# Performance work log

Measured on AMD Instinct MI355X. Metric: run time of the kernel, lower is better.

The kernel has to match this reference:

```python
import jax, jax.numpy as jnp
import numpy as np

B, S, T = 32, 64, 64          # batch, src_len, tgt_len
E, H, V = 512, 1024, 32000    # embed, hidden, vocab
WSCALE = 0.05                 # keep tanh/sigmoid in sane range


def setup_inputs() -> dict:
    key = jax.random.key(0)
    ks = jax.random.split(key, 14)
    n = lambda k, shp: jax.random.normal(k, shp, jnp.float32)
    return {
        "target": jax.random.randint(ks[0], (B, T), 0, V),
        "src_enc": n(ks[1], (B, S, 2 * H)),
        "h0": n(ks[2], (B, H)),
        "c0": n(ks[3], (B, H)),
        "emb": n(ks[4], (V, E)) * WSCALE,
        "W_ih": n(ks[5], (E, 4 * H)) * WSCALE,
        "W_hh": n(ks[6], (H, 4 * H)) * WSCALE,
        "b_rnn": jnp.zeros((4 * H,), jnp.float32),
        "W_attn": n(ks[7], (2 * H, H)) * WSCALE,
        "b_attn": jnp.zeros((H,), jnp.float32),
        "W_comb": n(ks[8], (2 * H, H)) * WSCALE,
        "b_comb": jnp.zeros((H,), jnp.float32),
        "W_out": n(ks[9], (H, V)) * WSCALE,
        "b_out": jnp.zeros((V,), jnp.float32),
    }


def reference(target, src_enc, h0, c0, emb, W_ih, W_hh, b_rnn,
              W_attn, b_attn, W_comb, b_comb, W_out, b_out):
    # Pre-project encoder states once (decode() applies attention.linear up front)
    enc_proj = src_enc @ W_attn + b_attn                 # [B,S,H]
    xs = emb[target[:, :-1]]                             # teacher forcing [B,T-1,E]
    xs = jnp.swapaxes(xs, 0, 1)                          # [T-1,B,E] for scan

    def step(carry, x_t):
        h, c = carry
        # LSTM cell (torch gate order i, f, g, o)
        gates = x_t @ W_ih + h @ W_hh + b_rnn            # [B,4H]
        i, f, g, o = jnp.split(gates, 4, axis=-1)
        c = jax.nn.sigmoid(f) * c + jax.nn.sigmoid(i) * jnp.tanh(g)
        h = jax.nn.sigmoid(o) * jnp.tanh(c)
        # Bilinear attention: score = h^T (W_attn e_s) over source positions
        scores = jnp.einsum('bsh,bh->bs', enc_proj, h)
        attn = jax.nn.softmax(scores, axis=-1)
        ctx = jnp.einsum('bs,bsh->bh', attn, enc_proj)   # [B,H]
        out = jnp.tanh(jnp.concatenate([h, ctx], axis=-1) @ W_comb + b_comb)
        return (h, c), out

    _, outs = jax.lax.scan(step, (h0, c0), xs)           # [T-1,B,H]
    outs = jnp.swapaxes(outs, 0, 1)                      # [B,T-1,H]
    logits = outs @ W_out + b_out                        # [B,T-1,V]
    return logits
```

## Files before the change

### kernel.cpp

```cpp
#include <hip/hip_runtime.h>
#include <stdint.h>

#define NB    32
#define NS    64
#define TDEC  63
#define NE    512
#define NH    1024
#define NV    32000

typedef float  floatx4 __attribute__((ext_vector_type(4)));
typedef short  short8  __attribute__((ext_vector_type(8)));
typedef short  short4v __attribute__((ext_vector_type(4)));

__device__ __forceinline__ float bf2f(short s) {
  return __uint_as_float(((uint32_t)(uint16_t)s) << 16);
}
__device__ __forceinline__ short f2bf(float f) {
  uint32_t u = __float_as_uint(f);
  uint32_t r = (u + 0x7fffu + ((u >> 16) & 1u)) >> 16;
  return (short)(uint16_t)r;
}
__device__ __forceinline__ float sigm(float x) { return 1.f / (1.f + expf(-x)); }

__device__ __forceinline__ int xcd_swz(int orig, int nwg) {
  return (orig & 7) * (nwg >> 3) + (orig >> 3);
}

__device__ __forceinline__ void tr_plain(
    const float* __restrict__ W, short* __restrict__ Wt, int K, int N,
    int bx, int by, int perm, float (*tile)[33], int tid)
{
  int k0 = bx * 32, n0 = by * 32;
  int tx = tid & 31, ty = tid >> 5;
#pragma unroll
  for (int r = 0; r < 32; r += 8)
    tile[ty + r][tx] = W[(size_t)(k0 + ty + r) * N + n0 + tx];
  __syncthreads();
  int kq = tid & 7, nl = tid >> 3;
  int n = n0 + nl;
  int rr = perm ? ((n & 1023) * 4 + (n >> 10)) : n;
  short4v v;
#pragma unroll
  for (int q = 0; q < 4; ++q) v[q] = f2bf(tile[kq * 4 + q][nl]);
  *(short4v*)&Wt[(size_t)rr * K + k0 + kq * 4] = v;
}

__device__ __forceinline__ void tr_split(
    const float* __restrict__ W, short* __restrict__ Wt_hi, short* __restrict__ Wt_lo,
    int K, int N, int bx, int by, int perm, float (*tile)[33], int tid)
{
  int k0 = bx * 32, n0 = by * 32;
  int tx = tid & 31, ty = tid >> 5;
#pragma unroll
  for (int r = 0; r < 32; r += 8)
    tile[ty + r][tx] = W[(size_t)(k0 + ty + r) * N + n0 + tx];
  __syncthreads();
  int kq = tid & 7, nl = tid >> 3;
  int n = n0 + nl;
  int rr = perm ? ((n & 1023) * 4 + (n >> 10)) : n;
  short4v vh, vl;
#pragma unroll
  for (int q = 0; q < 4; ++q) {
    float v = tile[kq * 4 + q][nl];
    short h = f2bf(v);
    vh[q] = h;
    vl[q] = f2bf(v - bf2f(h));
  }
  size_t o = (size_t)rr * K + k0 + kq * 4;
  *(short4v*)&Wt_hi[o] = vh;
  *(short4v*)&Wt_lo[o] = vl;
}

__global__ __launch_bounds__(256) void prep_all(
    const float* __restrict__ Wattn, const float* __restrict__ Wih,
    const float* __restrict__ Whh,
    const int* __restrict__ target,  const float* __restrict__ emb,
    const float* __restrict__ h0,    const float* __restrict__ c0,
    const float* __restrict__ brnn,  const float* __restrict__ src,
    short* __restrict__ WattnTh, short* __restrict__ WattnTl,
    short* __restrict__ WihTp,
    short* __restrict__ WhpHi,   short* __restrict__ WhpLo,
    short* __restrict__ xs, float* __restrict__ hf_all,
    short* __restrict__ hhi_all, short* __restrict__ hlo_all,
    float* __restrict__ c_buf, float* __restrict__ brnn_p,
    short* __restrict__ sAh, short* __restrict__ sAl)
{
  __shared__ float tile[32][33];
  const int blk = blockIdx.x;
  const int tid = threadIdx.x;

  if (blk < 2048) {
    tr_split(Wattn, WattnTh, WattnTl, 2048, 1024, blk & 63, blk >> 6, 0, tile, tid);
  } else if (blk < 4096) {
    int b = blk - 2048;
    tr_plain(Wih, WihTp, 512, 4096, b & 15, b >> 4, 1, tile, tid);
  } else if (blk < 8192) {
    int b = blk - 4096;
    tr_split(Whh, WhpHi, WhpLo, 1024, 4096, b & 31, b >> 5, 1, tile, tid);
  } else {
    const int NXS = TDEC * NB * NE;
    const int HN = NH * NB;
    const int NSRC = 2048 * 2048;
    int total = NXS + 2 * HN + 4096 + NSRC;
    int b = blk - 8192;
    for (int idx = b * 256 + tid; idx < total; idx += 2048 * 256) {
      if (idx < NXS) {
        int row = idx >> 9, e = idx & 511;
        int t = row >> 5, bb = row & 31;
        int token = target[bb * 64 + t];
        xs[idx] = f2bf(emb[(size_t)token * NE + e]);
      } else if (idx < NXS + HN) {
        int r = idx - NXS;
        float v = h0[r];
        hf_all[r] = v;
        short hh = f2bf(v);
        hhi_all[r] = hh;
        hlo_all[r] = f2bf(v - bf2f(hh));
      } else if (idx < NXS + 2 * HN) {
        int r = idx - NXS - HN;
        c_buf[r] = c0[r];
      } else if (idx < NXS + 2 * HN + 4096) {
        int c = idx - NXS - 2 * HN;
        brnn_p[c] = brnn[(c & 3) * 1024 + (c >> 2)];
      } else {
        int e = idx - NXS - 2 * HN - 4096;
        float v = src[e];
        short h = f2bf(v);
        sAh[e] = h;
        sAl[e] = f2bf(v - bf2f(h));
      }
    }
  }
}

template<int OUT_BF, int SWZ>
__global__ __launch_bounds__(256) void gemm_kernel(
    const short* __restrict__ Ab, const short* __restrict__ Bt,
    void* __restrict__ Cptr, const float* __restrict__ bias,
    int M, int N, int K)
{
  __shared__ char smem[2 * 128 * 72 * 2];
  short* As = (short*)smem;
  short* Bs = (short*)(smem + 128 * 72 * 2);
  float* cst = (float*)smem;
  int tile_id = blockIdx.y * gridDim.x + blockIdx.x;
  if (SWZ) tile_id = xcd_swz(tile_id, gridDim.x * gridDim.y);
  const int m0 = (tile_id % gridDim.x) * 128;
  const int n0 = (tile_id / gridDim.x) * 128;
  const int tid = threadIdx.x;
  const int lane = tid & 63;
  const int wid = tid >> 6;
  const int wr = wid >> 1, wc = wid & 1;

  floatx4 acc[4][4] = {};
  const int row = tid >> 1;
  const int ks  = (tid & 1) << 5;

  for (int k0 = 0; k0 < K; k0 += 64) {
    {
      int gm = m0 + row;
      short8 v0, v1, v2, v3;
      if (gm < M) {
        const short* src = Ab + (size_t)gm * K + k0 + ks;
        v0 = *(const short8*)src;
        v1 = *(const short8*)(src + 8);
        v2 = *(const short8*)(src + 16);
        v3 = *(const short8*)(src + 24);
      } else {
#pragma unroll
        for (int c = 0; c < 8; ++c) { v0[c] = 0; v1[c] = 0; v2[c] = 0; v3[c] = 0; }
      }
      *(short8*)&As[row * 72 + ks]      = v0;
      *(short8*)&As[row * 72 + ks + 8]  = v1;
      *(short8*)&As[row * 72 + ks + 16] = v2;
      *(short8*)&As[row * 72 + ks + 24] = v3;
    }
    {
      const short* src = Bt + (size_t)(n0 + row) * K + k0 + ks;
      *(short8*)&Bs[row * 72 + ks]      = *(const short8*)src;
      *(short8*)&Bs[row * 72 + ks + 8]  = *(const short8*)(src + 8);
      *(short8*)&Bs[row * 72 + ks + 16] = *(const short8*)(src + 16);
      *(short8*)&Bs[row * 72 + ks + 24] = *(const short8*)(src + 24);
    }
    __syncthreads();

    const int kA = (lane >> 4) << 3;
    const int rsel = lane & 15;
#pragma unroll
    for (int kk = 0; kk < 64; kk += 32) {
      short8 af[4], bfr[4];
#pragma unroll
      for (int mi = 0; mi < 4; ++mi)
        af[mi] = *(const short8*)&As[(wr * 64 + mi * 16 + rsel) * 72 + kk + kA];
#pragma unroll
      for (int ni = 0; ni < 4; ++ni)
        bfr[ni] = *(const short8*)&Bs[(wc * 64 + ni * 16 + rsel) * 72 + kk + kA];
#pragma unroll
      for (int mi = 0; mi < 4; ++mi)
#pragma unroll
        for (int ni = 0; ni < 4; ++ni)
          acc[mi][ni] = __builtin_amdgcn_mfma_f32_16x16x32_bf16(af[mi], bfr[ni], acc[mi][ni], 0, 0, 0);
    }
    __syncthreads();
  }

  const int crow = (lane >> 4) * 4;
  const int ccol = lane & 15;
  if (OUT_BF) {
#pragma unroll
    for (int mi = 0; mi < 4; ++mi) {
#pragma unroll
      for (int ni = 0; ni < 4; ++ni) {
        int gn = n0 + wc * 64 + ni * 16 + ccol;
        float bv = bias[gn];
#pragma unroll
        for (int i = 0; i < 4; ++i) {
          int gm = m0 + wr * 64 + mi * 16 + crow + i;
          if (gm < M)
            __builtin_nontemporal_store(f2bf(acc[mi][ni][i] + bv),
                                        &((short*)Cptr)[(size_t)gm * N + gn]);
        }
      }
    }
  } else {
#pragma unroll
    for (int p = 0; p < 4; ++p) {
      __syncthreads();
      if (wr == (p >> 1)) {
        int mi0 = (p & 1) * 2;
#pragma unroll
        for (int mm = 0; mm < 2; ++mm) {
#pragma unroll
          for (int ni = 0; ni < 4; ++ni) {
            int c = wc * 64 + ni * 16 + ccol;
#pragma unroll
            for (int i = 0; i < 4; ++i)
              cst[(mm * 16 + crow + i) * 132 + c] = acc[mi0 + mm][ni][i];
          }
        }
      }
      __syncthreads();
#pragma unroll
      for (int rep = 0; rep < 4; ++rep) {
        int cell = tid + rep * 256;
        int r = cell >> 5, q = cell & 31;
        int gm = m0 + p * 32 + r;
        int gn = n0 + q * 4;
        if (gm < M) {
          float4 bv = *(const float4*)&bias[gn];
          floatx4 v;
          v[0] = cst[r * 132 + q * 4 + 0] + bv.x;
          v[1] = cst[r * 132 + q * 4 + 1] + bv.y;
          v[2] = cst[r * 132 + q * 4 + 2] + bv.z;
          v[3] = cst[r * 132 + q * 4 + 3] + bv.w;
          __builtin_nontemporal_store(v, (floatx4*)&((float*)Cptr)[(size_t)gm * N + gn]);
        }
      }
    }
  }
}

__global__ __launch_bounds__(256) void gemm_pre(
    const short* __restrict__ Ah, const short* __restrict__ Al,
    const short* __restrict__ Bt_hi, const short* __restrict__ Bt_lo,
    float* __restrict__ Cenc, const float* __restrict__ battn,
    const short* __restrict__ Ag, const short* __restrict__ Btg,
    short* __restrict__ Cg, const float* __restrict__ brnn_p)
{
  __shared__ char smem[4 * 128 * 72 * 2];
  const int tid = threadIdx.x;
  const int lane = tid & 63;
  const int wid = tid >> 6;
  const int wr = wid >> 1, wc = wid & 1;
  const int row = tid >> 1;
  const int ks  = (tid & 1) << 5;
  const int kA = (lane >> 4) << 3;
  const int rsel = lane & 15;
  const int crow = (lane >> 4) * 4;
  const int ccol = lane & 15;

  if (blockIdx.x < 128) {
    short* As_hi = (short*)smem;
    short* As_lo = (short*)(smem + 1 * 128 * 72 * 2);
    short* Bs_hi = (short*)(smem + 2 * 128 * 72 * 2);
    short* Bs_lo = (short*)(smem + 3 * 128 * 72 * 2);
    const int K = 2048, N = NH;
    int tile_id = xcd_swz(blockIdx.x, 128);
    const int m0 = (tile_id % 16) * 128;
    const int n0 = (tile_id / 16) * 128;

    floatx4 acc[4][4] = {};
    for (int k0 = 0; k0 < K; k0 += 64) {
      {
        size_t o = (size_t)(m0 + row) * K + k0 + ks;
#pragma unroll
        for (int c = 0; c < 4; ++c) {
          *(short8*)&As_hi[row * 72 + ks + c * 8] = *(const short8*)(Ah + o + c * 8);
          *(short8*)&As_lo[row * 72 + ks + c * 8] = *(const short8*)(Al + o + c * 8);
        }
      }
      {
        size_t o = (size_t)(n0 + row) * K + k0 + ks;
#pragma unroll
        for (int c = 0; c < 4; ++c) {
          *(short8*)&Bs_hi[row * 72 + ks + c * 8] = *(const short8*)(Bt_hi + o + c * 8);
          *(short8*)&Bs_lo[row * 72 + ks + c * 8] = *(const short8*)(Bt_lo + o + c * 8);
        }
      }
      __syncthreads();
#pragma unroll
      for (int kk = 0; kk < 64; kk += 32) {
        short8 ah[4], al[4], bh[4], bl[4];
#pragma unroll
        for (int mi = 0; mi < 4; ++mi) {
          int off = (wr * 64 + mi * 16 + rsel) * 72 + kk + kA;
          ah[mi] = *(const short8*)&As_hi[off];
          al[mi] = *(const short8*)&As_lo[off];
        }
#pragma unroll
        for (int ni = 0; ni < 4; ++ni) {
          int off = (wc * 64 + ni * 16 + rsel) * 72 + kk + kA;
          bh[ni] = *(const short8*)&Bs_hi[off];
          bl[ni] = *(const short8*)&Bs_lo[off];
        }
#pragma unroll
        for (int mi = 0; mi < 4; ++mi)
#pragma unroll
          for (int ni = 0; ni < 4; ++ni) {
            floatx4 a = acc[mi][ni];
            a = __builtin_amdgcn_mfma_f32_16x16x32_bf16(al[mi], bh[ni], a, 0, 0, 0);
            a = __builtin_amdgcn_mfma_f32_16x16x32_bf16(ah[mi], bl[ni], a, 0, 0, 0);
            a = __builtin_amdgcn_mfma_f32_16x16x32_bf16(ah[mi], bh[ni], a, 0, 0, 0);
            acc[mi][ni] = a;
          }
      }
      __syncthreads();
    }
#pragma unroll
    for (int mi = 0; mi < 4; ++mi) {
#pragma unroll
      for (int ni = 0; ni < 4; ++ni) {
        int gn = n0 + wc * 64 + ni * 16 + ccol;
        float bv = battn[gn];
#pragma unroll
        for (int i = 0; i < 4; ++i) {
          int gm = m0 + wr * 64 + mi * 16 + crow + i;
          Cenc[(size_t)gm * N + gn] = acc[mi][ni][i] + bv;
        }
      }
    }
  } else {
    short* As = (short*)smem;
    short* Bs = (short*)(smem + 128 * 72 * 2);
    const int K = NE, N = 4096, M = TDEC * NB;
    int tile_id = xcd_swz(blockIdx.x - 128, 512);
    const int m0 = (tile_id % 16) * 128;
    const int n0 = (tile_id / 16) * 128;

    floatx4 acc[4][4] = {};
    for (int k0 = 0; k0 < K; k0 += 64) {
      {
        int gm = m0 + row;
        short8 v0, v1, v2, v3;
        if (gm < M) {
          const short* src = Ag + (size_t)gm * K + k0 + ks;
          v0 = *(const short8*)src;
          v1 = *(const short8*)(src + 8);
          v2 = *(const short8*)(src + 16);
          v3 = *(const short8*)(src + 24);
        } else {
#pragma unroll
          for (int c = 0; c < 8; ++c) { v0[c] = 0; v1[c] = 0; v2[c] = 0; v3[c] = 0; }
        }
        *(short8*)&As[row * 72 + ks]      = v0;
        *(short8*)&As[row * 72 + ks + 8]  = v1;
        *(short8*)&As[row * 72 + ks + 16] = v2;
        *(short8*)&As[row * 72 + ks + 24] = v3;
      }
      {
        const short* src = Btg + (size_t)(n0 + row) * K + k0 + ks;
        *(short8*)&Bs[row * 72 + ks]      = *(const short8*)src;
        *(short8*)&Bs[row * 72 + ks + 8]  = *(const short8*)(src + 8);
        *(short8*)&Bs[row * 72 + ks + 16] = *(const short8*)(src + 16);
        *(short8*)&Bs[row * 72 + ks + 24] = *(const short8*)(src + 24);
      }
      __syncthreads();
#pragma unroll
      for (int kk = 0; kk < 64; kk += 32) {
        short8 af[4], bfr[4];
#pragma unroll
        for (int mi = 0; mi < 4; ++mi)
          af[mi] = *(const short8*)&As[(wr * 64 + mi * 16 + rsel) * 72 + kk + kA];
#pragma unroll
        for (int ni = 0; ni < 4; ++ni)
          bfr[ni] = *(const short8*)&Bs[(wc * 64 + ni * 16 + rsel) * 72 + kk + kA];
#pragma unroll
        for (int mi = 0; mi < 4; ++mi)
#pragma unroll
          for (int ni = 0; ni < 4; ++ni)
            acc[mi][ni] = __builtin_amdgcn_mfma_f32_16x16x32_bf16(af[mi], bfr[ni], acc[mi][ni], 0, 0, 0);
      }
      __syncthreads();
    }
#pragma unroll
    for (int mi = 0; mi < 4; ++mi) {
#pragma unroll
      for (int ni = 0; ni < 4; ++ni) {
        int gn = n0 + wc * 64 + ni * 16 + ccol;
        float bv = brnn_p[gn];
#pragma unroll
        for (int i = 0; i < 4; ++i) {
          int gm = m0 + wr * 64 + mi * 16 + crow + i;
          if (gm < M)
            __builtin_nontemporal_store(f2bf(acc[mi][ni][i] + bv),
                                        &Cg[(size_t)gm * N + gn]);
        }
      }
    }
  }
}

__global__ __launch_bounds__(512) void scan_a(
    int t,
    const short* __restrict__ Whp_hi,
    const short* __restrict__ Whp_lo,
    const short* __restrict__ gatesx,
    short* __restrict__ hhi_all,
    short* __restrict__ hlo_all,
    float* __restrict__ hf_all,
    float* __restrict__ c_buf,
    const float* __restrict__ Wout,  short* __restrict__ WoutT,
    const float* __restrict__ Wcomb, short* __restrict__ WcTHi,
    short* __restrict__ WcTLo)
{
  __shared__ float smem[8 * 32 * 33];
  const int blk = blockIdx.x;
  const int tid = threadIdx.x;

  if (blk >= 128) {
    float (*tile)[33] = (float(*)[33])smem;
    if (blk < 636) {
      int id = t * 508 + (blk - 128);
      if (id < 32000) {
        int k0 = (id & 31) * 32, n0 = (id >> 5) * 32;
        if (tid < 256) {
          int tx = tid & 31, ty = tid >> 5;
#pragma unroll
          for (int r = 0; r < 32; r += 8)
            tile[ty + r][tx] = Wout[(size_t)(k0 + ty + r) * 32000 + n0 + tx];
        }
        __syncthreads();
        if (tid < 256) {
          int kq = tid & 7, nl = tid >> 3;
          int n = n0 + nl;
          short4v v;
#pragma unroll
          for (int q = 0; q < 4; ++q) v[q] = f2bf(tile[kq * 4 + q][nl]);
          *(short4v*)&WoutT[(size_t)n * 1024 + k0 + kq * 4] = v;
        }
      }
    } else {
      int id = t * 33 + (blk - 636);
      if (id < 2048) {
        int k0 = (id & 63) * 32, n0 = (id >> 6) * 32;
        if (tid < 256) {
          int tx = tid & 31, ty = tid >> 5;
#pragma unroll
          for (int r = 0; r < 32; r += 8)
            tile[ty + r][tx] = Wcomb[(size_t)(k0 + ty + r) * 1024 + n0 + tx];
        }
        __syncthreads();
        if (tid < 256) {
          int kq = tid & 7, nl = tid >> 3;
          int n = n0 + nl;
          short4v vh, vl;
#pragma unroll
          for (int q = 0; q < 4; ++q) {
            float v = tile[kq * 4 + q][nl];
            short h = f2bf(v);
            vh[q] = h;
            vl[q] = f2bf(v - bf2f(h));
          }
          size_t o = (size_t)n * 2048 + k0 + kq * 4;
          *(short4v*)&WcTHi[o] = vh;
          *(short4v*)&WcTLo[o] = vl;
        }
      }
    }
    return;
  }

  const int lane = tid & 63;
  const int wid = tid >> 6;
  const int rsel = lane & 15;
  const int kA = (lane >> 4) * 8;
  const int crow = (lane >> 4) * 4;
  const int ccol = lane & 15;

  const size_t spv = (size_t)t * (NH * NB);
  const size_t snw = (size_t)(t + 1) * (NH * NB);
  const short* Hh = hhi_all + spv;
  const short* Hl = hlo_all + spv;
  const int c0 = blk * 32;
  const int kb = wid * 128;

  floatx4 acc[2][2] = {};
  const short* wh0 = Whp_hi + (size_t)(c0 + rsel) * NH + kb + kA;
  const short* wl0 = Whp_lo + (size_t)(c0 + rsel) * NH + kb + kA;
  const short* wh1 = Whp_hi + (size_t)(c0 + 16 + rsel) * NH + kb + kA;
  const short* wl1 = Whp_lo + (size_t)(c0 + 16 + rsel) * NH + kb + kA;
  const short* ha0 = Hh + (size_t)rsel * NH + kb + kA;
  const short* la0 = Hl + (size_t)rsel * NH + kb + kA;
  const short* ha1 = Hh + (size_t)(16 + rsel) * NH + kb + kA;
  const short* la1 = Hl + (size_t)(16 + rsel) * NH + kb + kA;
#pragma unroll
  for (int kk = 0; kk < 4; ++kk) {
    int k0 = kk * 32;
    short8 a0h = *(const short8*)(ha0 + k0);
    short8 a0l = *(const short8*)(la0 + k0);
    short8 a1h = *(const short8*)(ha1 + k0);
    short8 a1l = *(const short8*)(la1 + k0);
    short8 b0h = *(const short8*)(wh0 + k0);
    short8 b0l = *(const short8*)(wl0 + k0);
    short8 b1h = *(const short8*)(wh1 + k0);
    short8 b1l = *(const short8*)(wl1 + k0);
    acc[0][0] = __builtin_amdgcn_mfma_f32_16x16x32_bf16(a0l, b0h, acc[0][0], 0, 0, 0);
    acc[0][0] = __builtin_amdgcn_mfma_f32_16x16x32_bf16(a0h, b0l, acc[0][0], 0, 0, 0);
    acc[0][0] = __builtin_amdgcn_mfma_f32_16x16x32_bf16(a0h, b0h, acc[0][0], 0, 0, 0);
    acc[0][1] = __builtin_amdgcn_mfma_f32_16x16x32_bf16(a0l, b1h, acc[0][1], 0, 0, 0);
    acc[0][1] = __builtin_amdgcn_mfma_f32_16x16x32_bf16(a0h, b1l, acc[0][1], 0, 0, 0);
    acc[0][1] = __builtin_amdgcn_mfma_f32_16x16x32_bf16(a0h, b1h, acc[0][1], 0, 0, 0);
    acc[1][0] = __builtin_amdgcn_mfma_f32_16x16x32_bf16(a1l, b0h, acc[1][0], 0, 0, 0);
    acc[1][0] = __builtin_amdgcn_mfma_f32_16x16x32_bf16(a1h, b0l, acc[1][0], 0, 0, 0);
    acc[1][0] = __builtin_amdgcn_mfma_f32_16x16x32_bf16(a1h, b0h, acc[1][0], 0, 0, 0);
    acc[1][1] = __builtin_amdgcn_mfma_f32_16x16x32_bf16(a1l, b1h, acc[1][1], 0, 0, 0);
    acc[1][1] = __builtin_amdgcn_mfma_f32_16x16x32_bf16(a1h, b1l, acc[1][1], 0, 0, 0);
    acc[1][1] = __builtin_amdgcn_mfma_f32_16x16x32_bf16(a1h, b1h, acc[1][1], 0, 0, 0);
  }
#pragma unroll
  for (int mi = 0; mi < 2; ++mi)
#pragma unroll
    for (int ni = 0; ni < 2; ++ni)
#pragma unroll
      for (int i = 0; i < 4; ++i)
        smem[wid * 1056 + (mi * 16 + crow + i) * 33 + ni * 16 + ccol] = acc[mi][ni][i];
  __syncthreads();
  if (tid < 256) {
    int b = tid & 31, jl = tid >> 5;
    float g[4];
#pragma unroll
    for (int q = 0; q < 4; ++q) {
      float s = 0;
#pragma unroll
      for (int w = 0; w < 8; ++w) s += smem[w * 1056 + b * 33 + jl * 4 + q];
      g[q] = s;
    }
    int jg = (c0 >> 2) + jl;
    const short* gx = gatesx + ((size_t)t * 32 + b) * 4096 + c0 + jl * 4;
    short4v gxv = *(const short4v*)gx;
    float gi = g[0] + bf2f(gxv[0]);
    float gf = g[1] + bf2f(gxv[1]);
    float gg = g[2] + bf2f(gxv[2]);
    float go = g[3] + bf2f(gxv[3]);
    float co = c_buf[b * NH + jg];
    float cn = sigm(gf) * co + sigm(gi) * tanhf(gg);
    float hn = sigm(go) * tanhf(cn);
    c_buf[b * NH + jg] = cn;
    hf_all[snw + b * NH + jg] = hn;
    short hh = f2bf(hn);
    hhi_all[snw + b * NH + jg] = hh;
    hlo_all[snw + b * NH + jg] = f2bf(hn - bf2f(hh));
  }
}

__global__ __launch_bounds__(256) void attn_batch(
    const float* __restrict__ encp,
    const float* __restrict__ hf_all,
    short* __restrict__ ctxhi_all,
    short* __restrict__ ctxlo_all)
{
  __shared__ float h_lds[NH];
  __shared__ float part[4 * 64];
  __shared__ float sc_lds[64];
  __shared__ float p_lds[64];
  const int blk = xcd_swz(blockIdx.x, gridDim.x);
  const int b = blk / TDEC;
  const int t = blk % TDEC;
  const int tid = threadIdx.x;
  const float* h = hf_all + ((size_t)(t + 1) * 32 + b) * NH;

  ((float4*)h_lds)[tid] = ((const float4*)h)[tid];
  __syncthreads();
  {
    int s = tid & 63, kc = tid >> 6;
    const float4* ep = (const float4*)(encp + ((size_t)(b * 64 + s)) * NH + kc * 256);
    const float4* hp = (const float4*)(h_lds + kc * 256);
    float ac0 = 0, ac1 = 0, ac2 = 0, ac3 = 0;
#pragma unroll
    for (int i = 0; i < 64; i += 4) {
      float4 e0 = ep[i],     h0v = hp[i];
      float4 e1 = ep[i + 1], h1v = hp[i + 1];
      float4 e2 = ep[i + 2], h2v = hp[i + 2];
      float4 e3 = ep[i + 3], h3v = hp[i + 3];
      ac0 = fmaf(e0.x, h0v.x, ac0); ac0 = fmaf(e0.y, h0v.y, ac0);
      ac0 = fmaf(e0.z, h0v.z, ac0); ac0 = fmaf(e0.w, h0v.w, ac0);
      ac1 = fmaf(e1.x, h1v.x, ac1); ac1 = fmaf(e1.y, h1v.y, ac1);
      ac1 = fmaf(e1.z, h1v.z, ac1); ac1 = fmaf(e1.w, h1v.w, ac1);
      ac2 = fmaf(e2.x, h2v.x, ac2); ac2 = fmaf(e2.y, h2v.y, ac2);
      ac2 = fmaf(e2.z, h2v.z, ac2); ac2 = fmaf(e2.w, h2v.w, ac2);
      ac3 = fmaf(e3.x, h3v.x, ac3); ac3 = fmaf(e3.y, h3v.y, ac3);
      ac3 = fmaf(e3.z, h3v.z, ac3); ac3 = fmaf(e3.w, h3v.w, ac3);
    }
    part[kc * 64 + s] = (ac0 + ac1) + (ac2 + ac3);
  }
  __syncthreads();
  if (tid < 64) {
    float sc = part[tid] + part[64 + tid] + part[128 + tid] + part[192 + tid];
    sc_lds[tid] = sc;
    float m = sc;
#pragma unroll
    for (int off = 32; off; off >>= 1) m = fmaxf(m, __shfl_xor(m, off));
    float e = expf(sc - m);
    float sum = e;
#pragma unroll
    for (int off = 32; off; off >>= 1) sum += __shfl_xor(sum, off);
    p_lds[tid] = e / sum;
  }
  __syncthreads();
  {
    int k4 = tid * 4;
    float a0 = 0, a1 = 0, a2 = 0, a3 = 0;
    const float* ep = encp + (size_t)(b * 64) * NH + k4;
    for (int s = 0; s < 64; ++s) {
      float p = p_lds[s];
      float4 e = *(const float4*)(ep + (size_t)s * NH);
      a0 = fmaf(p, e.x, a0); a1 = fmaf(p, e.y, a1);
      a2 = fmaf(p, e.z, a2); a3 = fmaf(p, e.w, a3);
    }
    size_t crow = ((size_t)t * 32 + b) * NH + k4;
    short4v c4h, c4l;
    float av[4] = {a0, a1, a2, a3};
#pragma unroll
    for (int q = 0; q < 4; ++q) {
      short hh = f2bf(av[q]);
      c4h[q] = hh;
      c4l[q] = f2bf(av[q] - bf2f(hh));
    }
    *(short4v*)(ctxhi_all + crow) = c4h;
    *(short4v*)(ctxlo_all + crow) = c4l;
  }
}

__global__ __launch_bounds__(256) void gemm_comb(
    const short* __restrict__ Ah_hi,
    const short* __restrict__ Ah_lo,
    const short* __restrict__ Cx_hi,
    const short* __restrict__ Cx_lo,
    const short* __restrict__ Bt_hi,
    const short* __restrict__ Bt_lo,
    const float* __restrict__ bcomb,
    short* __restrict__ outs)
{
  __shared__ short As_hi[128 * 72];
  __shared__ short As_lo[128 * 72];
  __shared__ short Bs_hi[128 * 72];
  __shared__ short Bs_lo[128 * 72];
  int tile_id = xcd_swz(blockIdx.y * gridDim.x + blockIdx.x, gridDim.x * gridDim.y);
  const int m0 = (tile_id % gridDim.x) * 128;
  const int n0 = (tile_id / gridDim.x) * 128;
  const int tid = threadIdx.x;
  const int lane = tid & 63;
  const int wid = tid >> 6;
  const int wr = wid >> 1, wc = wid & 1;

  floatx4 acc[4][4] = {};
  const int row = tid >> 1;
  const int ks  = (tid & 1) << 5;

  for (int k0 = 0; k0 < 2048; k0 += 64) {
    {
      int gr = m0 + row;
      const short* sh;
      const short* sl;
      if (k0 < NH) {
        sh = Ah_hi + (size_t)gr * NH + k0 + ks;
        sl = Ah_lo + (size_t)gr * NH + k0 + ks;
      } else {
        sh = Cx_hi + (size_t)gr * NH + (k0 - NH) + ks;
        sl = Cx_lo + (size_t)gr * NH + (k0 - NH) + ks;
      }
#pragma unroll
      for (int c = 0; c < 4; ++c) {
        *(short8*)&As_hi[row * 72 + ks + c * 8] = *(const short8*)(sh + c * 8);
        *(short8*)&As_lo[row * 72 + ks + c * 8] = *(const short8*)(sl + c * 8);
      }
    }
    {
      size_t o = (size_t)(n0 + row) * 2048 + k0 + ks;
#pragma unroll
      for (int c = 0; c < 4; ++c) {
        *(short8*)&Bs_hi[row * 72 + ks + c * 8] = *(const short8*)(Bt_hi + o + c * 8);
        *(short8*)&Bs_lo[row * 72 + ks + c * 8] = *(const short8*)(Bt_lo + o + c * 8);
      }
    }
    __syncthreads();

    const int kA = (lane >> 4) << 3;
    const int rsel = lane & 15;
#pragma unroll
    for (int kk = 0; kk < 64; kk += 32) {
      short8 ah[4], al[4], bh[4], bl[4];
#pragma unroll
      for (int mi = 0; mi < 4; ++mi) {
        int off = (wr * 64 + mi * 16 + rsel) * 72 + kk + kA;
        ah[mi] = *(const short8*)&As_hi[off];
        al[mi] = *(const short8*)&As_lo[off];
      }
#pragma unroll
      for (int ni = 0; ni < 4; ++ni) {
        int off = (wc * 64 + ni * 16 + rsel) * 72 + kk + kA;
        bh[ni] = *(const short8*)&Bs_hi[off];
        bl[ni] = *(const short8*)&Bs_lo[off];
      }
#pragma unroll
      for (int mi = 0; mi < 4; ++mi)
#pragma unroll
        for (int ni = 0; ni < 4; ++ni) {
          floatx4 a = acc[mi][ni];
          a = __builtin_amdgcn_mfma_f32_16x16x32_bf16(al[mi], bh[ni], a, 0, 0, 0);
          a = __builtin_amdgcn_mfma_f32_16x16x32_bf16(ah[mi], bl[ni], a, 0, 0, 0);
          a = __builtin_amdgcn_mfma_f32_16x16x32_bf16(ah[mi], bh[ni], a, 0, 0, 0);
          acc[mi][ni] = a;
        }
    }
    __syncthreads();
  }

  const int crow = (lane >> 4) * 4;
  const int ccol = lane & 15;
#pragma unroll
  for (int mi = 0; mi < 4; ++mi) {
#pragma unroll
    for (int ni = 0; ni < 4; ++ni) {
      int gn = n0 + wc * 64 + ni * 16 + ccol;
      float bv = bcomb[gn];
#pragma unroll
      for (int i = 0; i < 4; ++i) {
        int gm = m0 + wr * 64 + mi * 16 + crow + i;
        if (gm < TDEC * NB) {
          int tt = gm >> 5, bb = gm & 31;
          outs[((size_t)bb * TDEC + tt) * NH + gn] = f2bf(tanhf(acc[mi][ni][i] + bv));
        }
      }
    }
  }
}

extern "C" void kernel_launch(void* const* d_in, const int* in_sizes, int n_in,
                              void* d_out, int out_size, void* d_ws, size_t ws_size,
                              hipStream_t stream)
{
  const int*   target = (const int*)  d_in[0];
  const float* src    = (const float*)d_in[1];
  const float* h0     = (const float*)d_in[2];
  const float* c0     = (const float*)d_in[3];
  const float* emb    = (const float*)d_in[4];
  const float* Wih    = (const float*)d_in[5];
  const float* Whh    = (const float*)d_in[6];
  const float* brnn   = (const float*)d_in[7];
  const float* Wattn  = (const float*)d_in[8];
  const float* battn  = (const float*)d_in[9];
  const float* Wcomb  = (const float*)d_in[10];
  const float* bcomb  = (const float*)d_in[11];
  const float* Wout   = (const float*)d_in[12];
  const float* bout   = (const float*)d_in[13];
  float* out = (float*)d_out;

  char* ws = (char*)d_ws;
  size_t off = 0;
  auto take = [&](size_t bytes) { char* p = ws + off; off += (bytes + 255) & ~(size_t)255; return p; };
  short* WoutT    = (short*)take((size_t)NV * NH * 2);
  short* WattnTh  = (short*)take((size_t)NH * 2048 * 2);
  short* WattnTl  = (short*)take((size_t)NH * 2048 * 2);
  short* WihTp    = (short*)take((size_t)4096 * NE * 2);
  short* WhpHi    = (short*)take((size_t)4096 * NH * 2);
  short* WhpLo    = (short*)take((size_t)4096 * NH * 2);
  short* WcTHi    = (short*)take((size_t)NH * 2048 * 2);
  short* WcTLo    = (short*)take((size_t)NH * 2048 * 2);
  short* xs_bf    = (short*)take((size_t)TDEC * NB * NE * 2);
  float* encp     = (float*)take((size_t)NB * NS * NH * 4);
  short* gatesx   = (short*)take((size_t)TDEC * NB * 4096 * 2);
  short* outs_bf  = (short*)take((size_t)TDEC * NB * NH * 2);
  float* hf_all   = (float*)take((size_t)65 * NB * NH * 4);
  short* hhi_all  = (short*)take((size_t)65 * NB * NH * 2);
  short* hlo_all  = (short*)take((size_t)65 * NB * NH * 2);
  short* ctxhi_a  = (short*)take((size_t)2048 * NH * 2);
  short* ctxlo_a  = (short*)take((size_t)2048 * NH * 2);
  float* c_buf    = (float*)take((size_t)NH * NB * 4);
  float* brnn_p   = (float*)take((size_t)4096 * 4);
  short* sAl      = (short*)take((size_t)2048 * 2048 * 2);
  short* sAh      = (short*)take((size_t)2048 * 2048 * 2);
  if (off > ws_size) return;

  prep_all<<<10240, 256, 0, stream>>>(
      Wattn, Wih, Whh, target, emb, h0, c0, brnn, src,
      WattnTh, WattnTl, WihTp, WhpHi, WhpLo,
      xs_bf, hf_all, hhi_all, hlo_all, c_buf, brnn_p, sAh, sAl);
  gemm_pre<<<640, 256, 0, stream>>>(
      sAh, sAl, WattnTh, WattnTl, encp, battn,
      xs_bf, WihTp, gatesx, brnn_p);
  for (int t = 0; t < TDEC; ++t)
    scan_a<<<669, 512, 0, stream>>>(t, WhpHi, WhpLo, gatesx, hhi_all, hlo_all,
                                    hf_all, c_buf, Wout, WoutT, Wcomb, WcTHi, WcTLo);
  attn_batch<<<TDEC * NB, 256, 0, stream>>>(encp, hf_all, ctxhi_a, ctxlo_a);
  gemm_comb<<<dim3(16, 8), 256, 0, stream>>>(hhi_all + (size_t)32 * NH, hlo_all + (size_t)32 * NH,
                                             ctxhi_a, ctxlo_a, WcTHi, WcTLo, bcomb, outs_bf);
  gemm_kernel<0, 1><<<dim3(16, NV / 128), 256, 0, stream>>>(outs_bf, WoutT, out, bout, TDEC * NB, NV, NH);
}
```

Before: 1.137 ms.

## Fuse attention into scan launches, lagging one step behind the LSTM recurrence

Removes the separate batched attention kernel and computes each step's attention in 32 extra blocks of the scan launch, using the hidden state from the previous launch (t-1). An extra 64th launch finishes the last attention step. The aim is to hide attention work inside the latency-bound serial scan launches, where many CUs sit idle. In exchange it adds one more kernel launch, and the attention blocks now compete with the recurrence blocks in every step.

```diff
diff --git a/kernel.cpp b/kernel.cpp
--- a/kernel.cpp
+++ b/kernel.cpp
@@ -431,16 +431,91 @@
     float* __restrict__ c_buf,
     const float* __restrict__ Wout,  short* __restrict__ WoutT,
     const float* __restrict__ Wcomb, short* __restrict__ WcTHi,
-    short* __restrict__ WcTLo)
+    short* __restrict__ WcTLo,
+    const float* __restrict__ encp,
+    short* __restrict__ ctxhi_all,
+    short* __restrict__ ctxlo_all)
 {
   __shared__ float smem[8 * 32 * 33];
   const int blk = blockIdx.x;
   const int tid = threadIdx.x;
 
-  if (blk >= 128) {
+  if (blk >= 128 && blk < 160) {
+    const int ta = t - 1;
+    if (ta < 0 || ta >= TDEC) return;
+    const int b = blk - 128;
+    float* h_lds  = smem;
+    float* part   = smem + 1024;
+    float* sc_lds = smem + 1280;
+    float* p_lds  = smem + 1344;
+    const float* h = hf_all + ((size_t)(ta + 1) * 32 + b) * NH;
+    if (tid < 256) ((float4*)h_lds)[tid] = ((const float4*)h)[tid];
+    __syncthreads();
+    if (tid < 256) {
+      int s = tid & 63, kc = tid >> 6;
+      const float4* ep = (const float4*)(encp + ((size_t)(b * 64 + s)) * NH + kc * 256);
+      const float4* hp = (const float4*)(h_lds + kc * 256);
+      float ac0 = 0, ac1 = 0, ac2 = 0, ac3 = 0;
+#pragma unroll
+      for (int i = 0; i < 64; i += 4) {
+        float4 e0 = ep[i],     h0v = hp[i];
+        float4 e1 = ep[i + 1], h1v = hp[i + 1];
+        float4 e2 = ep[i + 2], h2v = hp[i + 2];
+        float4 e3 = ep[i + 3], h3v = hp[i + 3];
+        ac0 = fmaf(e0.x, h0v.x, ac0); ac0 = fmaf(e0.y, h0v.y, ac0);
+        ac0 = fmaf(e0.z, h0v.z, ac0); ac0 = fmaf(e0.w, h0v.w, ac0);
+        ac1 = fmaf(e1.x, h1v.x, ac1); ac1 = fmaf(e1.y, h1v.y, ac1);
+        ac1 = fmaf(e1.z, h1v.z, ac1); ac1 = fmaf(e1.w, h1v.w, ac1);
+        ac2 = fmaf(e2.x, h2v.x, ac2); ac2 = fmaf(e2.y, h2v.y, ac2);
+        ac2 = fmaf(e2.z, h2v.z, ac2); ac2 = fmaf(e2.w, h2v.w, ac2);
+        ac3 = fmaf(e3.x, h3v.x, ac3); ac3 = fmaf(e3.y, h3v.y, ac3);
+        ac3 = fmaf(e3.z, h3v.z, ac3); ac3 = fmaf(e3.w, h3v.w, ac3);
+      }
+      part[kc * 64 + s] = (ac0 + ac1) + (ac2 + ac3);
+    }
+    __syncthreads();
+    if (tid < 64) {
+      float sc = part[tid] + part[64 + tid] + part[128 + tid] + part[192 + tid];
+      sc_lds[tid] = sc;
+      float m = sc;
+#pragma unroll
+      for (int off = 32; off; off >>= 1) m = fmaxf(m, __shfl_xor(m, off));
+      float e = expf(sc - m);
+      float sum = e;
+#pragma unroll
+      for (int off = 32; off; off >>= 1) sum += __shfl_xor(sum, off);
+      p_lds[tid] = e / sum;
+    }
+    __syncthreads();
+    if (tid < 256) {
+      int k4 = tid * 4;
+      float a0 = 0, a1 = 0, a2 = 0, a3 = 0;
+      const float* ep = encp + (size_t)(b * 64) * NH + k4;
+      for (int s = 0; s < 64; ++s) {
+        float p = p_lds[s];
+        float4 e = *(const float4*)(ep + (size_t)s * NH);
+        a0 = fmaf(p, e.x, a0); a1 = fmaf(p, e.y, a1);
+        a2 = fmaf(p, e.z, a2); a3 = fmaf(p, e.w, a3);
+      }
+      size_t crow2 = ((size_t)ta * 32 + b) * NH + k4;
+      short4v c4h, c4l;
+      float av[4] = {a0, a1, a2, a3};
+#pragma unroll
+      for (int q = 0; q < 4; ++q) {
+        short hh = f2bf(av[q]);
+        c4h[q] = hh;
+        c4l[q] = f2bf(av[q] - bf2f(hh));
+      }
+      *(short4v*)(ctxhi_all + crow2) = c4h;
+      *(short4v*)(ctxlo_all + crow2) = c4l;
+    }
+    return;
+  }
+
+  if (blk >= 160) {
     float (*tile)[33] = (float(*)[33])smem;
-    if (blk < 636) {
-      int id = t * 508 + (blk - 128);
+    if (blk < 668) {
+      int id = t * 508 + (blk - 160);
       if (id < 32000) {
         int k0 = (id & 31) * 32, n0 = (id >> 5) * 32;
         if (tid < 256) {
@@ -460,7 +535,7 @@
         }
       }
     } else {
-      int id = t * 33 + (blk - 636);
+      int id = t * 33 + (blk - 668);
       if (id < 2048) {
         int k0 = (id & 63) * 32, n0 = (id >> 6) * 32;
         if (tid < 256) {
@@ -490,6 +565,7 @@
     return;
   }
 
+  if (t >= TDEC) return;
   const int lane = tid & 63;
   const int wid = tid >> 6;
   const int rsel = lane & 15;
@@ -570,84 +646,6 @@
     short hh = f2bf(hn);
     hhi_all[snw + b * NH + jg] = hh;
     hlo_all[snw + b * NH + jg] = f2bf(hn - bf2f(hh));
-  }
-}
-
-__global__ __launch_bounds__(256) void attn_batch(
-    const float* __restrict__ encp,
-    const float* __restrict__ hf_all,
-    short* __restrict__ ctxhi_all,
-    short* __restrict__ ctxlo_all)
-{
-  __shared__ float h_lds[NH];
-  __shared__ float part[4 * 64];
-  __shared__ float sc_lds[64];
-  __shared__ float p_lds[64];
-  const int blk = xcd_swz(blockIdx.x, gridDim.x);
-  const int b = blk / TDEC;
-  const int t = blk % TDEC;
-  const int tid = threadIdx.x;
-  const float* h = hf_all + ((size_t)(t + 1) * 32 + b) * NH;
-
-  ((float4*)h_lds)[tid] = ((const float4*)h)[tid];
-  __syncthreads();
-  {
-    int s = tid & 63, kc = tid >> 6;
-    const float4* ep = (const float4*)(encp + ((size_t)(b * 64 + s)) * NH + kc * 256);
-    const float4* hp = (const float4*)(h_lds + kc * 256);
-    float ac0 = 0, ac1 = 0, ac2 = 0, ac3 = 0;
-#pragma unroll
-    for (int i = 0; i < 64; i += 4) {
-      float4 e0 = ep[i],     h0v = hp[i];
-      float4 e1 = ep[i + 1], h1v = hp[i + 1];
-      float4 e2 = ep[i + 2], h2v = hp[i + 2];
-      float4 e3 = ep[i + 3], h3v = hp[i + 3];
-      ac0 = fmaf(e0.x, h0v.x, ac0); ac0 = fmaf(e0.y, h0v.y, ac0);
-      ac0 = fmaf(e0.z, h0v.z, ac0); ac0 = fmaf(e0.w, h0v.w, ac0);
-      ac1 = fmaf(e1.x, h1v.x, ac1); ac1 = fmaf(e1.y, h1v.y, ac1);
-      ac1 = fmaf(e1.z, h1v.z, ac1); ac1 = fmaf(e1.w, h1v.w, ac1);
-      ac2 = fmaf(e2.x, h2v.x, ac2); ac2 = fmaf(e2.y, h2v.y, ac2);
-      ac2 = fmaf(e2.z, h2v.z, ac2); ac2 = fmaf(e2.w, h2v.w, ac2);
-      ac3 = fmaf(e3.x, h3v.x, ac3); ac3 = fmaf(e3.y, h3v.y, ac3);
-      ac3 = fmaf(e3.z, h3v.z, ac3); ac3 = fmaf(e3.w, h3v.w, ac3);
-    }
-    part[kc * 64 + s] = (ac0 + ac1) + (ac2 + ac3);
-  }
-  __syncthreads();
-  if (tid < 64) {
-    float sc = part[tid] + part[64 + tid] + part[128 + tid] + part[192 + tid];
-    sc_lds[tid] = sc;
-    float m = sc;
-#pragma unroll
-    for (int off = 32; off; off >>= 1) m = fmaxf(m, __shfl_xor(m, off));
-    float e = expf(sc - m);
-    float sum = e;
-#pragma unroll
-    for (int off = 32; off; off >>= 1) sum += __shfl_xor(sum, off);
-    p_lds[tid] = e / sum;
-  }
-  __syncthreads();
-  {
-    int k4 = tid * 4;
-    float a0 = 0, a1 = 0, a2 = 0, a3 = 0;
-    const float* ep = encp + (size_t)(b * 64) * NH + k4;
-    for (int s = 0; s < 64; ++s) {
-      float p = p_lds[s];
-      float4 e = *(const float4*)(ep + (size_t)s * NH);
-      a0 = fmaf(p, e.x, a0); a1 = fmaf(p, e.y, a1);
-      a2 = fmaf(p, e.z, a2); a3 = fmaf(p, e.w, a3);
-    }
-    size_t crow = ((size_t)t * 32 + b) * NH + k4;
-    short4v c4h, c4l;
-    float av[4] = {a0, a1, a2, a3};
-#pragma unroll
-    for (int q = 0; q < 4; ++q) {
-      short hh = f2bf(av[q]);
-      c4h[q] = hh;
-      c4l[q] = f2bf(av[q] - bf2f(hh));
-    }
-    *(short4v*)(ctxhi_all + crow) = c4h;
-    *(short4v*)(ctxlo_all + crow) = c4l;
   }
 }
 
@@ -809,10 +807,10 @@
   gemm_pre<<<640, 256, 0, stream>>>(
       sAh, sAl, WattnTh, WattnTl, encp, battn,
       xs_bf, WihTp, gatesx, brnn_p);
-  for (int t = 0; t < TDEC; ++t)
-    scan_a<<<669, 512, 0, stream>>>(t, WhpHi, WhpLo, gatesx, hhi_all, hlo_all,
-                                    hf_all, c_buf, Wout, WoutT, Wcomb, WcTHi, WcTLo);
-  attn_batch<<<TDEC * NB, 256, 0, stream>>>(encp, hf_all, ctxhi_a, ctxlo_a);
+  for (int t = 0; t < TDEC + 1; ++t)
+    scan_a<<<701, 512, 0, stream>>>(t, WhpHi, WhpLo, gatesx, hhi_all, hlo_all,
+                                    hf_all, c_buf, Wout, WoutT, Wcomb, WcTHi, WcTLo,
+                                    encp, ctxhi_a, ctxlo_a);
   gemm_comb<<<dim3(16, 8), 256, 0, stream>>>(hhi_all + (size_t)32 * NH, hlo_all + (size_t)32 * NH,
                                              ctxhi_a, ctxlo_a, WcTHi, WcTLo, bcomb, outs_bf);
   gemm_kernel<0, 1><<<dim3(16, NV / 128), 256, 0, stream>>>(outs_bf, WoutT, out, bout, TDEC * NB, NV, NH);
```

Result: slower. 1.352 ms (+18.9%).
